# Performance work log

Measured on AMD Instinct MI355X. Metric: run time of the kernel, lower is better.

## Reference

```python
import jax, jax.numpy as jnp
import numpy as np

N_NODES = 100000  # size_u + size_v + size_w
N_MP = 3          # metapaths vv, uu, ww
N_EDGES = 1000000
D_IN = 64
D_OUT = 64


def setup_inputs() -> dict:
    key = jax.random.key(0)
    k1, k2, k3, k4 = jax.random.split(key, 4)
    x = jax.random.normal(k1, (N_NODES, D_IN), dtype=jnp.float32)
    # per-metapath GCNConv weight (glorot-ish scale)
    W = jax.random.normal(k2, (N_MP, D_IN, D_OUT), dtype=jnp.float32) * (1.0 / np.sqrt(D_IN))
    edge_index = jax.random.randint(k3, (N_MP, 2, N_EDGES), 0, N_NODES, dtype=jnp.int64)
    edge_weight = jax.random.uniform(k4, (N_MP, N_EDGES), dtype=jnp.float32)
    return {"x": x, "W": W, "edge_index": edge_index, "edge_weight": edge_weight}


def _gcn_conv(x, w_mat, row, col, ew, num_nodes):
    # gcn_norm without self-loops: deg[i] = sum of edge weights into i
    deg = jax.ops.segment_sum(ew, col, num_segments=num_nodes)
    dinv = jnp.where(deg > 0, jax.lax.rsqrt(jnp.where(deg > 0, deg, 1.0)), 0.0)
    norm = dinv[row] * ew * dinv[col]          # [E]
    h = x @ w_mat                               # [N, D_OUT]
    msg = h[row] * norm[:, None]                # [E, D_OUT] gather + scale
    return jax.ops.segment_sum(msg, col, num_segments=num_nodes)  # scatter-add


def reference(x, W, edge_index, edge_weight):
    num_nodes = x.shape[0]
    outs = []
    for i in range(N_MP):  # small fixed loop over structurally distinct encoders
        row = edge_index[i, 0]
        col = edge_index[i, 1]
        out = _gcn_conv(x, W[i], row, col, edge_weight[i], num_nodes)
        outs.append(jax.nn.relu(out))  # act=nn.ReLU
    return jnp.stack(outs)  # [3, N, D_OUT]; dropout omitted (eval mode)
```

## Files before the change

### kernel.cpp

```cpp
#include <hip/hip_runtime.h>
#include <hip/hip_fp16.h>

#define NNODES 100000
#define NMP 3
#define NEDGES 1000000
#define D 64
#define NTOT (NMP * NNODES)
#define BINW 1024
#define NBIN 293
#define CAPB 10944
#define T1 3072
#define OVCAP 131072

typedef __attribute__((ext_vector_type(8))) short bf16x8;
typedef __attribute__((ext_vector_type(4))) float floatx4;

__device__ __forceinline__ unsigned short f2bf(float f) {
    unsigned u = __float_as_uint(f);
    u = (u + 0x7FFFu + ((u >> 16) & 1u)) >> 16;
    return (unsigned short)u;
}
__device__ __forceinline__ __half2 u2h(unsigned u) {
    __half2 r;
    *reinterpret_cast<unsigned*>(&r) = u;
    return r;
}

__global__ __launch_bounds__(512) void split_kernel(const int* __restrict__ ei,
                                                    const float* __restrict__ ew,
                                                    int* __restrict__ gcur,
                                                    int* __restrict__ ovcur,
                                                    int* __restrict__ ovf,
                                                    uint2* __restrict__ A) {
    __shared__ int hist[NBIN], cur[NBIN];
    const int t = threadIdx.x;
    const int mp = blockIdx.y;
    const int e0 = blockIdx.x * T1;
    for (int i = t; i < NBIN; i += 512) hist[i] = 0;
    __syncthreads();
    unsigned key[6]; float w[6]; int bn[6];
#pragma unroll
    for (int i = 0; i < 6; ++i) {
        int e = e0 + i * 512 + t;
        bn[i] = -1;
        if (e < NEDGES) {
            int r = ei[(mp * 2 + 0) * NEDGES + e];
            int c = ei[(mp * 2 + 1) * NEDGES + e];
            w[i] = ew[mp * NEDGES + e];
            int cflat = mp * NNODES + c;
            int rflat = mp * NNODES + r;
            int b = cflat >> 10;
            bn[i] = b;
            key[i] = ((unsigned)(cflat & 1023) << 19) | (unsigned)rflat;
            atomicAdd(&hist[b], 1);
        }
    }
    __syncthreads();
    for (int i = t; i < NBIN; i += 512) {
        int v = hist[i];
        cur[i] = v ? atomicAdd(&gcur[i], v) : 0;
    }
    __syncthreads();
#pragma unroll
    for (int i = 0; i < 6; ++i) {
        if (bn[i] >= 0) {
            int pos = atomicAdd(&cur[bn[i]], 1);
            if (pos < CAPB) {
                A[(size_t)bn[i] * CAPB + pos] = make_uint2(key[i], __float_as_uint(w[i]));
            } else {
                int op = atomicAdd(ovcur, 1);
                if (op < OVCAP) {
                    int cflat = (bn[i] << 10) | (int)(key[i] >> 19);
                    ovf[3 * op] = cflat;
                    ovf[3 * op + 1] = (int)(key[i] & 0x7FFFFu);
                    ovf[3 * op + 2] = __float_as_int(w[i]);
                }
            }
        }
    }
}

__global__ __launch_bounds__(256) void compact2_kernel(const int* __restrict__ gcur,
                                                       const uint2* __restrict__ A,
                                                       const int* __restrict__ ovcur,
                                                       const int* __restrict__ ovf,
                                                       uint2* __restrict__ C,
                                                       int2* __restrict__ nodeoff,
                                                       float* __restrict__ dinv) {
    const int bin = blockIdx.x;
    __shared__ int cnt[BINW];
    __shared__ float wsum[BINW];
    __shared__ int pos[BINW];
    __shared__ int sh[256];
    const int t = threadIdx.x;
    for (int i = t; i < BINW; i += 256) { cnt[i] = 0; wsum[i] = 0.0f; }
    __syncthreads();
    const int len = min(gcur[bin], CAPB);
    const uint2* Ab = A + (size_t)bin * CAPB;
    for (int p = t; p < len; p += 256) {
        uint2 rec = Ab[p];
        atomicAdd(&cnt[rec.x >> 19], 1);
        atomicAdd(&wsum[rec.x >> 19], __uint_as_float(rec.y));
    }
    const int ovn = min(*ovcur, OVCAP);
    for (int i = t; i < ovn; i += 256) {
        int cflat = ovf[3 * i];
        if ((cflat >> 10) == bin) {
            atomicAdd(&cnt[cflat & 1023], 1);
            atomicAdd(&wsum[cflat & 1023], __int_as_float(ovf[3 * i + 2]));
        }
    }
    __syncthreads();
    int c0 = cnt[4 * t], c1 = cnt[4 * t + 1], c2 = cnt[4 * t + 2], c3 = cnt[4 * t + 3];
    int vsum = c0 + c1 + c2 + c3;
    sh[t] = vsum;
    __syncthreads();
    for (int d = 1; d < 256; d <<= 1) {
        int add = (t >= d) ? sh[t - d] : 0;
        __syncthreads();
        sh[t] += add;
        __syncthreads();
    }
    const int base = bin * CAPB;
    const int lim = base + CAPB;
    int p0 = base + sh[t] - vsum;
    int p1 = p0 + c0, p2 = p1 + c1, p3 = p2 + c2;
    pos[4 * t] = p0; pos[4 * t + 1] = p1; pos[4 * t + 2] = p2; pos[4 * t + 3] = p3;
    int starts[4] = {p0, p1, p2, p3};
    int cs[4] = {c0, c1, c2, c3};
#pragma unroll
    for (int j = 0; j < 4; ++j) {
        int cl = 4 * t + j;
        int node = (bin << 10) + cl;
        if (node < NTOT) {
            nodeoff[node] = make_int2(starts[j], cs[j]);
            float dg = wsum[cl];
            dinv[node] = (dg > 0.0f) ? rsqrtf(dg) : 0.0f;
        }
    }
    __syncthreads();
    for (int p = t; p < len; p += 256) {
        uint2 rec = Ab[p];
        int s = atomicAdd(&pos[rec.x >> 19], 1);
        if (s < lim) C[s] = make_uint2(rec.x & 0x7FFFFu, rec.y);
    }
    for (int i = t; i < ovn; i += 256) {
        int cflat = ovf[3 * i];
        if ((cflat >> 10) == bin) {
            int s = atomicAdd(&pos[cflat & 1023], 1);
            if (s < lim) C[s] = make_uint2((unsigned)ovf[3 * i + 1], (unsigned)ovf[3 * i + 2]);
        }
    }
}

__global__ __launch_bounds__(256) void prep_w_kernel(const float* __restrict__ W,
                                                     unsigned short* __restrict__ wT) {
    int idx = blockIdx.x * 256 + threadIdx.x;
    if (idx >= NMP * D * D) return;
    int mp = idx >> 12, rem = idx & 4095;
    int k = rem >> 6, n = rem & 63;
    wT[(mp * D + n) * D + k] = f2bf(W[idx]);
}

__global__ __launch_bounds__(256) void gemm_kernel(const float* __restrict__ x,
                                                   const unsigned short* __restrict__ wT,
                                                   const float* __restrict__ dinv,
                                                   unsigned short* __restrict__ h) {
    const int wave = threadIdx.x >> 6;
    const int lane = threadIdx.x & 63;
    const int rowbase = (blockIdx.x * 4 + wave) * 16;
    if (rowbase >= NNODES) return;
    const int m = lane & 15;
    const int q = lane >> 4;
    const float4* xr = (const float4*)(x + (size_t)(rowbase + m) * D);
    bf16x8 a[2];
#pragma unroll
    for (int kc = 0; kc < 2; ++kc) {
        float4 x0 = xr[kc * 8 + q * 2];
        float4 x1 = xr[kc * 8 + q * 2 + 1];
        a[kc][0] = f2bf(x0.x); a[kc][1] = f2bf(x0.y);
        a[kc][2] = f2bf(x0.z); a[kc][3] = f2bf(x0.w);
        a[kc][4] = f2bf(x1.x); a[kc][5] = f2bf(x1.y);
        a[kc][6] = f2bf(x1.z); a[kc][7] = f2bf(x1.w);
    }
#pragma unroll
    for (int mp = 0; mp < NMP; ++mp) {
        float dv = dinv[mp * NNODES + rowbase + m];
#pragma unroll
        for (int nt = 0; nt < 4; ++nt) {
            const bf16x8* bp = (const bf16x8*)(wT + (size_t)(mp * D + nt * 16 + m) * D);
            bf16x8 b0 = bp[q];
            bf16x8 b1 = bp[4 + q];
            floatx4 acc = {0.f, 0.f, 0.f, 0.f};
            acc = __builtin_amdgcn_mfma_f32_16x16x32_bf16(b0, a[0], acc, 0, 0, 0);
            acc = __builtin_amdgcn_mfma_f32_16x16x32_bf16(b1, a[1], acc, 0, 0, 0);
            unsigned v0 = (unsigned)__half_as_ushort(__float2half(acc[0] * dv)) |
                          ((unsigned)__half_as_ushort(__float2half(acc[1] * dv)) << 16);
            unsigned v1 = (unsigned)__half_as_ushort(__float2half(acc[2] * dv)) |
                          ((unsigned)__half_as_ushort(__float2half(acc[3] * dv)) << 16);
            *(uint2*)(h + ((size_t)mp * NNODES + rowbase + m) * D + nt * 16 + q * 4) =
                make_uint2(v0, v1);
        }
    }
}

__global__ __launch_bounds__(256) void gather_kernel(const int2* __restrict__ nodeoff,
                                                     const uint2* __restrict__ dense,
                                                     const unsigned short* __restrict__ h,
                                                     const float* __restrict__ dinv,
                                                     float* __restrict__ out) {
    const int tid = threadIdx.x;
    const int wave = tid >> 6, lane = tid & 63;
    const int sub = lane >> 5;
    const int g = (lane >> 3) & 3;
    const int f = lane & 7;
    const int w = blockIdx.x * 8 + wave * 2 + sub;
    int2 off = nodeoff[w];
    const int start = off.x, end = off.x + off.y;
    const uint4* hp = (const uint4*)h;
    __half2 acc2[4];
    acc2[0] = __float2half2_rn(0.0f); acc2[1] = __float2half2_rn(0.0f);
    acc2[2] = __float2half2_rn(0.0f); acc2[3] = __float2half2_rn(0.0f);
    if (end > start) {
        const int last = end - 1;
        uint2 prA = dense[min(start + g, last)];
        uint2 prB = dense[min(start + 4 + g, last)];
        uint4 hvA = hp[(size_t)prA.x * 8 + f];
        for (int p = start; p < end; p += 4) {
            uint2 prC = dense[min(p + 8 + g, last)];
            uint4 hvB = hp[(size_t)prB.x * 8 + f];
            float wgt = (p + g < end) ? __uint_as_float(prA.y) : 0.0f;
            __half2 wp = __float2half2_rn(wgt);
            acc2[0] = __hfma2(u2h(hvA.x), wp, acc2[0]);
            acc2[1] = __hfma2(u2h(hvA.y), wp, acc2[1]);
            acc2[2] = __hfma2(u2h(hvA.z), wp, acc2[2]);
            acc2[3] = __hfma2(u2h(hvA.w), wp, acc2[3]);
            prA = prB; hvA = hvB; prB = prC;
        }
    }
    float acc[8];
    acc[0] = __low2float(acc2[0]); acc[1] = __high2float(acc2[0]);
    acc[2] = __low2float(acc2[1]); acc[3] = __high2float(acc2[1]);
    acc[4] = __low2float(acc2[2]); acc[5] = __high2float(acc2[2]);
    acc[6] = __low2float(acc2[3]); acc[7] = __high2float(acc2[3]);
#pragma unroll
    for (int j = 0; j < 8; ++j) {
        acc[j] += __shfl_xor(acc[j], 8);
        acc[j] += __shfl_xor(acc[j], 16);
    }
    float dv = dinv[w];
    if (g < 2) {
        float4 o = g ? make_float4(acc[4], acc[5], acc[6], acc[7])
                     : make_float4(acc[0], acc[1], acc[2], acc[3]);
        o.x = fmaxf(o.x * dv, 0.0f);
        o.y = fmaxf(o.y * dv, 0.0f);
        o.z = fmaxf(o.z * dv, 0.0f);
        o.w = fmaxf(o.w * dv, 0.0f);
        ((float4*)out)[(size_t)w * 16 + f * 2 + g] = o;
    }
}

extern "C" void kernel_launch(void* const* d_in, const int* in_sizes, int n_in,
                              void* d_out, int out_size, void* d_ws, size_t ws_size,
                              hipStream_t stream) {
    const float* x  = (const float*)d_in[0];
    const float* W  = (const float*)d_in[1];
    const int*   ei = (const int*)d_in[2];
    const float* ew = (const float*)d_in[3];
    float* out = (float*)d_out;

    char* ws = (char*)d_ws;
    uint2* A           = (uint2*)(ws + 0);
    unsigned short* h  = (unsigned short*)(ws + 0);
    uint2* C           = (uint2*)(ws + 38400000);
    int2*  nodeoff     = (int2*)(ws + 64052736);
    float* dinv        = (float*)(ws + 66452736);
    unsigned short* wT = (unsigned short*)(ws + 67652736);
    int*   gcur        = (int*)(ws + 67677312);
    int*   ovcur       = (int*)(ws + 67678484);
    int*   ovf         = (int*)(ws + 67678488);

    hipMemsetAsync(gcur, 0, 1176, stream);

    split_kernel<<<dim3((NEDGES + T1 - 1) / T1, NMP), 512, 0, stream>>>(ei, ew, gcur,
                                                                        ovcur, ovf, A);
    compact2_kernel<<<NBIN, 256, 0, stream>>>(gcur, A, ovcur, ovf, C, nodeoff, dinv);
    prep_w_kernel<<<(NMP * D * D + 255) / 256, 256, 0, stream>>>(W, wT);
    gemm_kernel<<<(NNODES / 16 + 3) / 4, 256, 0, stream>>>(x, wT, dinv, h);
    gather_kernel<<<NTOT / 8, 256, 0, stream>>>(nodeoff, C, h, dinv, out);
}
```

Before: 285.0 us.

## Stage split records in LDS sorted by bin for coalesced global writes

The split kernel now counting-sorts each block's edge records in shared memory using a block-wide prefix scan over the bin histogram. It then writes them to the global bin buckets in consecutive runs instead of scattering each record individually. Records per block also rise from 3072 to 5632 (11 per thread), which lengthens the contiguous runs and cuts the number of global atomics on bin cursors. The costs are more shared memory (about 57KB), which lowers occupancy, extra barriers for the scan, and more registers per thread.

```diff
diff --git a/kernel.cpp b/kernel.cpp
--- a/kernel.cpp
+++ b/kernel.cpp
@@ -9,7 +9,8 @@
 #define BINW 1024
 #define NBIN 293
 #define CAPB 10944
-#define T1 3072
+#define T1 5632
+#define RPT 11
 #define OVCAP 131072
 
 typedef __attribute__((ext_vector_type(8))) short bf16x8;
@@ -32,15 +33,19 @@
                                                     int* __restrict__ ovcur,
                                                     int* __restrict__ ovf,
                                                     uint2* __restrict__ A) {
-    __shared__ int hist[NBIN], cur[NBIN];
+    __shared__ uint2 stage[T1];
+    __shared__ unsigned short sbin[T1];
+    __shared__ int hist[NBIN], lbase[NBIN], gbase[NBIN], lcur[NBIN];
+    __shared__ int sh[512];
     const int t = threadIdx.x;
     const int mp = blockIdx.y;
     const int e0 = blockIdx.x * T1;
+    const int nrec = min(T1, NEDGES - e0);
     for (int i = t; i < NBIN; i += 512) hist[i] = 0;
     __syncthreads();
-    unsigned key[6]; float w[6]; int bn[6];
-#pragma unroll
-    for (int i = 0; i < 6; ++i) {
+    unsigned key[RPT]; float w[RPT]; int bn[RPT];
+#pragma unroll
+    for (int i = 0; i < RPT; ++i) {
         int e = e0 + i * 512 + t;
         bn[i] = -1;
         if (e < NEDGES) {
@@ -56,25 +61,44 @@
         }
     }
     __syncthreads();
-    for (int i = t; i < NBIN; i += 512) {
-        int v = hist[i];
-        cur[i] = v ? atomicAdd(&gcur[i], v) : 0;
-    }
-    __syncthreads();
-#pragma unroll
-    for (int i = 0; i < 6; ++i) {
+    int v = (t < NBIN) ? hist[t] : 0;
+    sh[t] = v;
+    __syncthreads();
+    for (int d = 1; d < 512; d <<= 1) {
+        int add = (t >= d) ? sh[t - d] : 0;
+        __syncthreads();
+        sh[t] += add;
+        __syncthreads();
+    }
+    if (t < NBIN) {
+        int ex = sh[t] - v;
+        lbase[t] = ex;
+        lcur[t] = ex;
+        gbase[t] = v ? atomicAdd(&gcur[t], v) : 0;
+    }
+    __syncthreads();
+#pragma unroll
+    for (int i = 0; i < RPT; ++i) {
         if (bn[i] >= 0) {
-            int pos = atomicAdd(&cur[bn[i]], 1);
-            if (pos < CAPB) {
-                A[(size_t)bn[i] * CAPB + pos] = make_uint2(key[i], __float_as_uint(w[i]));
-            } else {
-                int op = atomicAdd(ovcur, 1);
-                if (op < OVCAP) {
-                    int cflat = (bn[i] << 10) | (int)(key[i] >> 19);
-                    ovf[3 * op] = cflat;
-                    ovf[3 * op + 1] = (int)(key[i] & 0x7FFFFu);
-                    ovf[3 * op + 2] = __float_as_int(w[i]);
-                }
+            int s = atomicAdd(&lcur[bn[i]], 1);
+            stage[s] = make_uint2(key[i], __float_as_uint(w[i]));
+            sbin[s] = (unsigned short)bn[i];
+        }
+    }
+    __syncthreads();
+    for (int s = t; s < nrec; s += 512) {
+        int b = sbin[s];
+        uint2 rec = stage[s];
+        int pos = gbase[b] + (s - lbase[b]);
+        if (pos < CAPB) {
+            A[(size_t)b * CAPB + pos] = rec;
+        } else {
+            int op = atomicAdd(ovcur, 1);
+            if (op < OVCAP) {
+                int cflat = (b << 10) | (int)(rec.x >> 19);
+                ovf[3 * op] = cflat;
+                ovf[3 * op + 1] = (int)(rec.x & 0x7FFFFu);
+                ovf[3 * op + 2] = (int)rec.y;
             }
         }
     }
```

After: 285.6 us. About the same (+0.2%).

## Replace bin-split CSR build with global-atomic histogram, scan, scatter

Applied to the files above, without the earlier changes.

Replaces the two-pass bin split and per-bin compaction with three kernels. The first builds per-node counts and degree sums with global atomics, the second runs a per-bin prefix scan that writes node offsets, cursors and dinv, and the third scatters each edge straight into its CSR slot with a global atomic cursor. Overflow edges are now handled in the gather kernel by a linear scan of the overflow list. This removes the intermediate bin buffer and one full pass over it. In exchange it adds heavy global atomic contention, including float atomics on wsum, reads the edge arrays twice, scatters writes randomly, and makes gather cost grow with the overflow count.

```diff
diff --git a/kernel.cpp b/kernel.cpp
--- a/kernel.cpp
+++ b/kernel.cpp
@@ -8,8 +8,8 @@
 #define NTOT (NMP * NNODES)
 #define BINW 1024
 #define NBIN 293
+#define NPAD (NBIN * BINW)
 #define CAPB 10944
-#define T1 3072
 #define OVCAP 131072
 
 typedef __attribute__((ext_vector_type(8))) short bf16x8;
@@ -25,130 +25,107 @@
     *reinterpret_cast<unsigned*>(&r) = u;
     return r;
 }
-
-__global__ __launch_bounds__(512) void split_kernel(const int* __restrict__ ei,
-                                                    const float* __restrict__ ew,
-                                                    int* __restrict__ gcur,
-                                                    int* __restrict__ ovcur,
-                                                    int* __restrict__ ovf,
-                                                    uint2* __restrict__ A) {
-    __shared__ int hist[NBIN], cur[NBIN];
+__device__ __forceinline__ float h2f_lo(unsigned u) {
+    return __half2float(__ushort_as_half((unsigned short)(u & 0xFFFFu)));
+}
+__device__ __forceinline__ float h2f_hi(unsigned u) {
+    return __half2float(__ushort_as_half((unsigned short)(u >> 16)));
+}
+
+__device__ __forceinline__ int block_excl_scan(int v, int t, int nthreads, int* wsums) {
+    const int lane = t & 63, wv = t >> 6;
+    int s = v;
+#pragma unroll
+    for (int d = 1; d < 64; d <<= 1) {
+        int u = __shfl_up(s, d);
+        if (lane >= d) s += u;
+    }
+    if (lane == 63) wsums[wv] = s;
+    __syncthreads();
+    if (wv == 0) {
+        const int nw = nthreads >> 6;
+        int ws = (lane < nw) ? wsums[lane] : 0;
+#pragma unroll
+        for (int d = 1; d < 8; d <<= 1) {
+            int u = __shfl_up(ws, d);
+            if (lane >= d) ws += u;
+        }
+        if (lane < nw) wsums[lane] = ws;
+    }
+    __syncthreads();
+    int wbase = wv ? wsums[wv - 1] : 0;
+    return wbase + s - v;
+}
+
+__global__ __launch_bounds__(256) void hist_kernel(const int* __restrict__ ei,
+                                                   const float* __restrict__ ew,
+                                                   int* __restrict__ cnt,
+                                                   float* __restrict__ wsum) {
+    const int mp = blockIdx.y;
+    int e = blockIdx.x * 1024 + threadIdx.x;
+#pragma unroll
+    for (int i = 0; i < 4; ++i, e += 256) {
+        if (e < NEDGES) {
+            int c = ei[(mp * 2 + 1) * NEDGES + e];
+            float w = ew[mp * NEDGES + e];
+            int cflat = mp * NNODES + c;
+            atomicAdd(&cnt[cflat], 1);
+            __hip_atomic_fetch_add(&wsum[cflat], w, __ATOMIC_RELAXED,
+                                   __HIP_MEMORY_SCOPE_AGENT);
+        }
+    }
+}
+
+__global__ __launch_bounds__(512) void scan_kernel(const int* __restrict__ cnt,
+                                                   const float* __restrict__ wsum,
+                                                   int2* __restrict__ nodeoff,
+                                                   int* __restrict__ pcur,
+                                                   float* __restrict__ dinv) {
+    const int bin = blockIdx.x;
+    __shared__ int wsums[8];
     const int t = threadIdx.x;
+    const int n0 = (bin << 10) + 2 * t, n1 = n0 + 1;
+    int c0 = cnt[n0], c1 = cnt[n1];
+    int ex = block_excl_scan(c0 + c1, t, 512, wsums);
+    const int base = bin * CAPB;
+    int s0 = base + ex, s1 = s0 + c0;
+    nodeoff[n0] = make_int2(s0, c0);
+    nodeoff[n1] = make_int2(s1, c1);
+    pcur[n0] = s0;
+    pcur[n1] = s1;
+    float d0 = wsum[n0], d1 = wsum[n1];
+    dinv[n0] = (d0 > 0.0f) ? rsqrtf(d0) : 0.0f;
+    dinv[n1] = (d1 > 0.0f) ? rsqrtf(d1) : 0.0f;
+}
+
+__global__ __launch_bounds__(256) void scatter_kernel(const int* __restrict__ ei,
+                                                      const float* __restrict__ ew,
+                                                      int* __restrict__ pcur,
+                                                      int* __restrict__ ovcur,
+                                                      int* __restrict__ ovf,
+                                                      uint2* __restrict__ C) {
     const int mp = blockIdx.y;
-    const int e0 = blockIdx.x * T1;
-    for (int i = t; i < NBIN; i += 512) hist[i] = 0;
-    __syncthreads();
-    unsigned key[6]; float w[6]; int bn[6];
-#pragma unroll
-    for (int i = 0; i < 6; ++i) {
-        int e = e0 + i * 512 + t;
-        bn[i] = -1;
+    int e = blockIdx.x * 1024 + threadIdx.x;
+#pragma unroll
+    for (int i = 0; i < 4; ++i, e += 256) {
         if (e < NEDGES) {
             int r = ei[(mp * 2 + 0) * NEDGES + e];
             int c = ei[(mp * 2 + 1) * NEDGES + e];
-            w[i] = ew[mp * NEDGES + e];
+            float w = ew[mp * NEDGES + e];
             int cflat = mp * NNODES + c;
             int rflat = mp * NNODES + r;
-            int b = cflat >> 10;
-            bn[i] = b;
-            key[i] = ((unsigned)(cflat & 1023) << 19) | (unsigned)rflat;
-            atomicAdd(&hist[b], 1);
-        }
-    }
-    __syncthreads();
-    for (int i = t; i < NBIN; i += 512) {
-        int v = hist[i];
-        cur[i] = v ? atomicAdd(&gcur[i], v) : 0;
-    }
-    __syncthreads();
-#pragma unroll
-    for (int i = 0; i < 6; ++i) {
-        if (bn[i] >= 0) {
-            int pos = atomicAdd(&cur[bn[i]], 1);
-            if (pos < CAPB) {
-                A[(size_t)bn[i] * CAPB + pos] = make_uint2(key[i], __float_as_uint(w[i]));
+            int slot = atomicAdd(&pcur[cflat], 1);
+            int binlim = ((cflat >> 10) + 1) * CAPB;
+            if (slot < binlim) {
+                C[slot] = make_uint2((unsigned)rflat, __float_as_uint(w));
             } else {
                 int op = atomicAdd(ovcur, 1);
                 if (op < OVCAP) {
-                    int cflat = (bn[i] << 10) | (int)(key[i] >> 19);
                     ovf[3 * op] = cflat;
-                    ovf[3 * op + 1] = (int)(key[i] & 0x7FFFFu);
-                    ovf[3 * op + 2] = __float_as_int(w[i]);
+                    ovf[3 * op + 1] = rflat;
+                    ovf[3 * op + 2] = __float_as_int(w);
                 }
             }
-        }
-    }
-}
-
-__global__ __launch_bounds__(256) void compact2_kernel(const int* __restrict__ gcur,
-                                                       const uint2* __restrict__ A,
-                                                       const int* __restrict__ ovcur,
-                                                       const int* __restrict__ ovf,
-                                                       uint2* __restrict__ C,
-                                                       int2* __restrict__ nodeoff,
-                                                       float* __restrict__ dinv) {
-    const int bin = blockIdx.x;
-    __shared__ int cnt[BINW];
-    __shared__ float wsum[BINW];
-    __shared__ int pos[BINW];
-    __shared__ int sh[256];
-    const int t = threadIdx.x;
-    for (int i = t; i < BINW; i += 256) { cnt[i] = 0; wsum[i] = 0.0f; }
-    __syncthreads();
-    const int len = min(gcur[bin], CAPB);
-    const uint2* Ab = A + (size_t)bin * CAPB;
-    for (int p = t; p < len; p += 256) {
-        uint2 rec = Ab[p];
-        atomicAdd(&cnt[rec.x >> 19], 1);
-        atomicAdd(&wsum[rec.x >> 19], __uint_as_float(rec.y));
-    }
-    const int ovn = min(*ovcur, OVCAP);
-    for (int i = t; i < ovn; i += 256) {
-        int cflat = ovf[3 * i];
-        if ((cflat >> 10) == bin) {
-            atomicAdd(&cnt[cflat & 1023], 1);
-            atomicAdd(&wsum[cflat & 1023], __int_as_float(ovf[3 * i + 2]));
-        }
-    }
-    __syncthreads();
-    int c0 = cnt[4 * t], c1 = cnt[4 * t + 1], c2 = cnt[4 * t + 2], c3 = cnt[4 * t + 3];
-    int vsum = c0 + c1 + c2 + c3;
-    sh[t] = vsum;
-    __syncthreads();
-    for (int d = 1; d < 256; d <<= 1) {
-        int add = (t >= d) ? sh[t - d] : 0;
-        __syncthreads();
-        sh[t] += add;
-        __syncthreads();
-    }
-    const int base = bin * CAPB;
-    const int lim = base + CAPB;
-    int p0 = base + sh[t] - vsum;
-    int p1 = p0 + c0, p2 = p1 + c1, p3 = p2 + c2;
-    pos[4 * t] = p0; pos[4 * t + 1] = p1; pos[4 * t + 2] = p2; pos[4 * t + 3] = p3;
-    int starts[4] = {p0, p1, p2, p3};
-    int cs[4] = {c0, c1, c2, c3};
-#pragma unroll
-    for (int j = 0; j < 4; ++j) {
-        int cl = 4 * t + j;
-        int node = (bin << 10) + cl;
-        if (node < NTOT) {
-            nodeoff[node] = make_int2(starts[j], cs[j]);
-            float dg = wsum[cl];
-            dinv[node] = (dg > 0.0f) ? rsqrtf(dg) : 0.0f;
-        }
-    }
-    __syncthreads();
-    for (int p = t; p < len; p += 256) {
-        uint2 rec = Ab[p];
-        int s = atomicAdd(&pos[rec.x >> 19], 1);
-        if (s < lim) C[s] = make_uint2(rec.x & 0x7FFFFu, rec.y);
-    }
-    for (int i = t; i < ovn; i += 256) {
-        int cflat = ovf[3 * i];
-        if ((cflat >> 10) == bin) {
-            int s = atomicAdd(&pos[cflat & 1023], 1);
-            if (s < lim) C[s] = make_uint2((unsigned)ovf[3 * i + 1], (unsigned)ovf[3 * i + 2]);
         }
     }
 }
@@ -208,6 +185,8 @@
                                                      const uint2* __restrict__ dense,
                                                      const unsigned short* __restrict__ h,
                                                      const float* __restrict__ dinv,
+                                                     const int* __restrict__ ovcur,
+                                                     const int* __restrict__ ovf,
                                                      float* __restrict__ out) {
     const int tid = threadIdx.x;
     const int wave = tid >> 6, lane = tid & 63;
@@ -250,6 +229,19 @@
     }
     float dv = dinv[w];
     if (g < 2) {
+        const int ovn = min(*ovcur, OVCAP);
+        if (ovn > 0) {
+            for (int i = 0; i < ovn; ++i) {
+                if (ovf[3 * i] == w) {
+                    float wgt = __int_as_float(ovf[3 * i + 2]);
+                    uint4 hv = hp[(size_t)ovf[3 * i + 1] * 8 + f];
+                    acc[0] += wgt * h2f_lo(hv.x); acc[1] += wgt * h2f_hi(hv.x);
+                    acc[2] += wgt * h2f_lo(hv.y); acc[3] += wgt * h2f_hi(hv.y);
+                    acc[4] += wgt * h2f_lo(hv.z); acc[5] += wgt * h2f_hi(hv.z);
+                    acc[6] += wgt * h2f_lo(hv.w); acc[7] += wgt * h2f_hi(hv.w);
+                }
+            }
+        }
         float4 o = g ? make_float4(acc[4], acc[5], acc[6], acc[7])
                      : make_float4(acc[0], acc[1], acc[2], acc[3]);
         o.x = fmaxf(o.x * dv, 0.0f);
@@ -270,22 +262,25 @@
     float* out = (float*)d_out;
 
     char* ws = (char*)d_ws;
-    uint2* A           = (uint2*)(ws + 0);
     unsigned short* h  = (unsigned short*)(ws + 0);
     uint2* C           = (uint2*)(ws + 38400000);
     int2*  nodeoff     = (int2*)(ws + 64052736);
-    float* dinv        = (float*)(ws + 66452736);
-    unsigned short* wT = (unsigned short*)(ws + 67652736);
-    int*   gcur        = (int*)(ws + 67677312);
-    int*   ovcur       = (int*)(ws + 67678484);
-    int*   ovf         = (int*)(ws + 67678488);
-
-    hipMemsetAsync(gcur, 0, 1176, stream);
-
-    split_kernel<<<dim3((NEDGES + T1 - 1) / T1, NMP), 512, 0, stream>>>(ei, ew, gcur,
-                                                                        ovcur, ovf, A);
-    compact2_kernel<<<NBIN, 256, 0, stream>>>(gcur, A, ovcur, ovf, C, nodeoff, dinv);
+    float* dinv        = (float*)(ws + 66452992);
+    unsigned short* wT = (unsigned short*)(ws + 67653120);
+    int*   cnt         = (int*)(ws + 67677696);
+    float* wsum        = (float*)(ws + 68877824);
+    int*   pcur        = (int*)(ws + 70077952);
+    int*   ovcur       = (int*)(ws + 71278080);
+    int*   ovf         = (int*)(ws + 71278084);
+
+    hipMemsetAsync(cnt, 0, 2400256, stream);
+    hipMemsetAsync(ovcur, 0, 4, stream);
+
+    dim3 egrid((NEDGES + 1023) / 1024, NMP);
+    hist_kernel<<<egrid, 256, 0, stream>>>(ei, ew, cnt, wsum);
+    scan_kernel<<<NBIN, 512, 0, stream>>>(cnt, wsum, nodeoff, pcur, dinv);
+    scatter_kernel<<<egrid, 256, 0, stream>>>(ei, ew, pcur, ovcur, ovf, C);
     prep_w_kernel<<<(NMP * D * D + 255) / 256, 256, 0, stream>>>(W, wT);
     gemm_kernel<<<(NNODES / 16 + 3) / 4, 256, 0, stream>>>(x, wT, dinv, h);
-    gather_kernel<<<NTOT / 8, 256, 0, stream>>>(nodeoff, C, h, dinv, out);
-}
+    gather_kernel<<<NTOT / 8, 256, 0, stream>>>(nodeoff, C, h, dinv, ovcur, ovf, out);
+}
```

Measured after the change: 716.4 us. +151.4%, slower.
